# Kernel optimization log

Measured on AMD Instinct MI355X. Metric: run time of the kernel, lower is better.

The kernel has to match this reference:

```python
import jax, jax.numpy as jnp
import numpy as np

NUM_USERS = 100000
NUM_ITEMS = 50000
NUM_EDGES = 1000000
H = 64            # initial embedding dim
DIMS = [64, 64]   # per-layer output dims
B = 16384         # BPR batch size
NEG_SLOPE = 0.2
EPS = 1e-12


def setup_inputs() -> dict:
    key = jax.random.key(0)
    ks = jax.random.split(key, 20)
    s = 1.0 / np.sqrt(H)
    inp = {
        'user_emb': jax.random.normal(ks[0], (NUM_USERS, H), jnp.float32) * 0.1,
        'item_emb': jax.random.normal(ks[1], (NUM_ITEMS, H), jnp.float32) * 0.1,
        'W1_0': jax.random.normal(ks[2], (H, DIMS[0]), jnp.float32) * s,
        'b1_0': jnp.zeros((DIMS[0],), jnp.float32),
        'W2_0': jax.random.normal(ks[3], (H, DIMS[0]), jnp.float32) * s,
        'b2_0': jnp.zeros((DIMS[0],), jnp.float32),
        'W1_1': jax.random.normal(ks[4], (DIMS[0], DIMS[1]), jnp.float32) * s,
        'b1_1': jnp.zeros((DIMS[1],), jnp.float32),
        'W2_1': jax.random.normal(ks[5], (DIMS[0], DIMS[1]), jnp.float32) * s,
        'b2_1': jnp.zeros((DIMS[1],), jnp.float32),
        'edge_index': jnp.stack([
            jax.random.randint(ks[6], (NUM_EDGES,), 0, NUM_USERS),
            jax.random.randint(ks[7], (NUM_EDGES,), 0, NUM_ITEMS),
        ], axis=0),
        'users': jax.random.randint(ks[8], (B,), 0, NUM_USERS),
        'pos_items': jax.random.randint(ks[9], (B,), 0, NUM_ITEMS),
        'neg_items': jax.random.randint(ks[10], (B,), 0, NUM_ITEMS),
    }
    return inp


def _edge_norm(src, dst):
    # symmetric sqrt-degree norm: (deg_src * deg_dst) ** -0.5 per edge
    ones = jnp.ones(src.shape[0], jnp.float32)
    du = jax.ops.segment_sum(ones, src, num_segments=NUM_USERS)[src]
    di = jax.ops.segment_sum(ones, dst, num_segments=NUM_ITEMS)[dst]
    return ((du * di) ** -0.5)[:, None]  # [E, 1]


def _epilogue(h):
    # leaky_relu(0.2) -> (dropout eval = identity) -> L2 row-normalize
    h = jnp.where(h >= 0, h, NEG_SLOPE * h)
    n = jnp.sqrt(jnp.sum(h * h, axis=1, keepdims=True))
    return h / jnp.maximum(n, EPS)


def _layer(u, i, src, dst, norm, W1, b1, W2, b2):
    # node-level W1 transform, gathered per edge (same math as per-edge W1(x_j))
    u1 = u @ W1 + b1            # [Nu, d]
    i1 = i @ W1 + b1            # [Ni, d]
    cross = u[src] * i[dst]     # [E, din]  shared by both directions
    mW2 = cross @ W2 + b2       # [E, d]
    # user -> item: x_j = user[src], aggregate at item dst
    out_i = jax.ops.segment_sum(norm * u1[src] + mW2, dst, num_segments=NUM_ITEMS)
    # item -> user: x_j = item[dst], aggregate at user src
    out_u = jax.ops.segment_sum(norm * i1[dst] + mW2, src, num_segments=NUM_USERS)
    return _epilogue(out_u), _epilogue(out_i)


def reference(user_emb, item_emb, W1_0, b1_0, W2_0, b2_0, W1_1, b1_1, W2_1, b2_1,
              edge_index, users, pos_items, neg_items):
    src, dst = edge_index[0], edge_index[1]
    norm = _edge_norm(src, dst)
    u_list, i_list = [user_emb], [item_emb]
    u, i = user_emb, item_emb
    u, i = _layer(u, i, src, dst, norm, W1_0, b1_0, W2_0, b2_0)
    u_list.append(u); i_list.append(i)
    u, i = _layer(u, i, src, dst, norm, W1_1, b1_1, W2_1, b2_1)
    u_list.append(u); i_list.append(i)
    user_all = jnp.concatenate(u_list, axis=1)   # [Nu, H+sum(DIMS)]
    item_all = jnp.concatenate(i_list, axis=1)   # [Ni, H+sum(DIMS)]
    return (user_all[users], item_all[pos_items], item_all[neg_items])
```

## Files before the change

### kernel.cpp

```cpp
#include <hip/hip_runtime.h>

#define NU 100000
#define NI 50000
#define NE 1000000
#define NB 16384

#define UB ((NU + 1023) / 1024)
#define IB ((NI + 1023) / 1024)

__global__ void deg_kernel(const int* __restrict__ ei, int* du, int* di) {
    int e = blockIdx.x * blockDim.x + threadIdx.x;
    if (e >= NE) return;
    atomicAdd(&du[ei[e]], 1);
    atomicAdd(&di[ei[NE + e]], 1);
}

__global__ __launch_bounds__(1024) void scan1_kernel(
        const int* __restrict__ du, const int* __restrict__ di,
        int* __restrict__ psum, float* __restrict__ rsd_u, float* __restrict__ rsd_i) {
    int b = blockIdx.x, tid = threadIdx.x;
    int v = 0;
    if (b < UB) {
        int i = b * 1024 + tid;
        if (i < NU) {
            int d = du[i]; v = d;
            rsd_u[i] = d > 0 ? 1.0f / sqrtf((float)d) : 0.f;
        }
    } else {
        int i = (b - UB) * 1024 + tid;
        if (i < NI) {
            int d = di[i]; v = d;
            rsd_i[i] = d > 0 ? 1.0f / sqrtf((float)d) : 0.f;
        }
    }
    int s = v;
    #pragma unroll
    for (int off = 32; off > 0; off >>= 1) s += __shfl_xor(s, off);
    __shared__ int ws[16];
    if ((tid & 63) == 0) ws[tid >> 6] = s;
    __syncthreads();
    if (tid == 0) {
        int t = 0;
        #pragma unroll
        for (int w = 0; w < 16; ++w) t += ws[w];
        psum[b] = t;
    }
}

__global__ __launch_bounds__(128) void scan2_kernel(int* __restrict__ psum) {
    int base = (blockIdx.x == 0) ? 0 : UB;
    int n = (blockIdx.x == 0) ? UB : IB;
    int tid = threadIdx.x;
    __shared__ int sh[128];
    int v = (tid < n) ? psum[base + tid] : 0;
    sh[tid] = v;
    __syncthreads();
    for (int off = 1; off < 128; off <<= 1) {
        int t = (tid >= off) ? sh[tid - off] : 0;
        __syncthreads();
        sh[tid] += t;
        __syncthreads();
    }
    if (tid < n) psum[base + tid] = sh[tid] - v;
}

__global__ __launch_bounds__(1024) void scan3_kernel(
        const int* __restrict__ du, const int* __restrict__ di,
        const int* __restrict__ psum,
        int* __restrict__ rp_u, int* __restrict__ rp_i,
        int* __restrict__ cur_u, int* __restrict__ cur_i) {
    int b = blockIdx.x, tid = threadIdx.x;
    const int* deg; int* rp; int* cur; int N; int i0;
    if (b < UB) { deg = du; rp = rp_u; cur = cur_u; N = NU; i0 = b * 1024; }
    else        { deg = di; rp = rp_i; cur = cur_i; N = NI; i0 = (b - UB) * 1024; }
    int i = i0 + tid;
    int v = (i < N) ? deg[i] : 0;
    __shared__ int sh[1024];
    sh[tid] = v;
    __syncthreads();
    for (int off = 1; off < 1024; off <<= 1) {
        int t = (tid >= off) ? sh[tid - off] : 0;
        __syncthreads();
        sh[tid] += t;
        __syncthreads();
    }
    int excl = sh[tid] - v + psum[b];
    if (i < N) { rp[i] = excl; cur[i] = excl; }
    if (b == 0 && tid == 0) { rp_u[NU] = NE; rp_i[NI] = NE; }
}

__global__ void fill_csr_kernel(const int* __restrict__ ei,
                                int* __restrict__ curu, int* __restrict__ curi,
                                int* __restrict__ csr_u, int* __restrict__ csr_i) {
    int e = blockIdx.x * blockDim.x + threadIdx.x;
    if (e >= NE) return;
    int s = ei[e], d = ei[NE + e];
    int si = atomicAdd(&curi[d], 1);
    csr_i[si] = s;
    int su = atomicAdd(&curu[s], 1);
    csr_u[su] = d;
}

__global__ __launch_bounds__(512) void gt_fused_kernel(
        const float* __restrict__ xu, const float* __restrict__ xi,
        const int* __restrict__ rpu, const int* __restrict__ rpi,
        const int* __restrict__ csru, const int* __restrict__ csri,
        const float* __restrict__ rsdu, const float* __restrict__ rsdi,
        const float* __restrict__ W1, const float* __restrict__ b1,
        const float* __restrict__ W2, const float* __restrict__ b2,
        float* __restrict__ outu, float* __restrict__ outi) {
    __shared__ float w1s[64 * 64];
    __shared__ float w2s[64 * 64];
    __shared__ float acs[8][128];
    int tid = threadIdx.x;
    #pragma unroll
    for (int t = 0; t < 8; ++t) {
        w1s[t * 512 + tid] = W1[t * 512 + tid];
        w2s[t * 512 + tid] = W2[t * 512 + tid];
    }
    __syncthreads();
    int wv = tid >> 6, lane = tid & 63;
    float b1v = b1[lane], b2v = b2[lane];
    const int NG = (NI + NU + 7) / 8;
    for (int g = blockIdx.x; g < NG; g += gridDim.x) {
        int n = g * 8 + wv;
        bool act = n < NI + NU;
        bool isItem = n < NI;
        int nn = isItem ? n : n - NI;
        const int* rp   = isItem ? rpi : rpu;
        const int* cs   = isItem ? csri : csru;
        const float* xin  = isItem ? xi : xu;
        const float* embo = isItem ? xu : xi;
        const float* rso  = isItem ? rsdu : rsdi;
        const float* rown = isItem ? rsdi : rsdu;
        float* outp = isItem ? outi : outu;

        float sp = 0.f, ss = 0.f, sw = 0.f, rs = 0.f, dgf = 0.f, xv = 0.f;
        if (act) {
            int beg = rp[nn], end = rp[nn + 1];
            dgf = (float)(end - beg);
            rs = rown[nn];
            xv = xin[nn * 64 + lane];
            int j = beg;
            for (; j + 3 < end; j += 4) {
                int i0 = cs[j], i1 = cs[j + 1], i2 = cs[j + 2], i3 = cs[j + 3];
                float w0 = rso[i0], w1v = rso[i1], w2v = rso[i2], w3v = rso[i3];
                float v0 = embo[i0 * 64 + lane];
                float v1 = embo[i1 * 64 + lane];
                float v2 = embo[i2 * 64 + lane];
                float v3 = embo[i3 * 64 + lane];
                sp += (v0 + v1) + (v2 + v3);
                ss += w0 * v0 + w1v * v1 + w2v * v2 + w3v * v3;
                sw += (w0 + w1v) + (w2v + w3v);
            }
            for (; j < end; ++j) {
                int i0 = cs[j];
                float w0 = rso[i0];
                float v0 = embo[i0 * 64 + lane];
                sp += v0; ss += w0 * v0; sw += w0;
            }
        }
        acs[wv][lane] = rs * ss;
        acs[wv][64 + lane] = xv * sp;
        if (act) {
            float acc = 0.f;
            #pragma unroll 8
            for (int k = 0; k < 64; ++k) {
                acc += acs[wv][k] * w1s[k * 64 + lane];
                acc += acs[wv][64 + k] * w2s[k * 64 + lane];
            }
            acc += rs * sw * b1v + dgf * b2v;
            float h = acc >= 0.f ? acc : 0.2f * acc;
            float nsq = h * h;
            #pragma unroll
            for (int off = 32; off > 0; off >>= 1) nsq += __shfl_xor(nsq, off);
            float nrm = sqrtf(nsq);
            outp[nn * 64 + lane] = h / fmaxf(nrm, 1e-12f);
        }
    }
}

__global__ void gather_kernel(const float* __restrict__ ue, const float* __restrict__ u1,
                              const float* __restrict__ u2, const float* __restrict__ ie,
                              const float* __restrict__ i1, const float* __restrict__ i2,
                              const int* __restrict__ users, const int* __restrict__ pos,
                              const int* __restrict__ neg, float* __restrict__ out) {
    int idx = blockIdx.x * blockDim.x + threadIdx.x;
    if (idx >= 3 * NB * 192) return;
    int which = idx / (NB * 192);
    int rem = idx - which * (NB * 192);
    int b = rem / 192, c = rem - b * 192;
    int seg = c >> 6, cc = c & 63;
    int row;
    const float* srcarr;
    if (which == 0) {
        row = users[b];
        srcarr = (seg == 0) ? ue : (seg == 1 ? u1 : u2);
    } else {
        row = (which == 1) ? pos[b] : neg[b];
        srcarr = (seg == 0) ? ie : (seg == 1 ? i1 : i2);
    }
    out[idx] = srcarr[(size_t)row * 64 + cc];
}

extern "C" void kernel_launch(void* const* d_in, const int* in_sizes, int n_in,
                              void* d_out, int out_size, void* d_ws, size_t ws_size,
                              hipStream_t stream) {
    const float* user_emb = (const float*)d_in[0];
    const float* item_emb = (const float*)d_in[1];
    const float* W1_0 = (const float*)d_in[2];
    const float* b1_0 = (const float*)d_in[3];
    const float* W2_0 = (const float*)d_in[4];
    const float* b2_0 = (const float*)d_in[5];
    const float* W1_1 = (const float*)d_in[6];
    const float* b1_1 = (const float*)d_in[7];
    const float* W2_1 = (const float*)d_in[8];
    const float* b2_1 = (const float*)d_in[9];
    const int* ei = (const int*)d_in[10];
    const int* users = (const int*)d_in[11];
    const int* pos = (const int*)d_in[12];
    const int* neg = (const int*)d_in[13];
    float* out = (float*)d_out;

    char* p = (char*)d_ws;
    int* du = (int*)p;        p += NU * 4;
    int* di = (int*)p;        p += NI * 4;
    float* rsd_u = (float*)p; p += NU * 4;
    float* rsd_i = (float*)p; p += NI * 4;
    int* psum = (int*)p;      p += (UB + IB) * 4;
    int* rp_u = (int*)p;      p += (NU + 1) * 4;
    int* rp_i = (int*)p;      p += (NI + 1) * 4;
    int* cur_u = (int*)p;     p += NU * 4;
    int* cur_i = (int*)p;     p += NI * 4;
    int* csr_u = (int*)p;     p += (size_t)NE * 4;
    int* csr_i = (int*)p;     p += (size_t)NE * 4;
    float* u1 = (float*)p;    p += (size_t)NU * 64 * 4;
    float* u2 = (float*)p;    p += (size_t)NU * 64 * 4;
    float* i1 = (float*)p;    p += (size_t)NI * 64 * 4;
    float* i2 = (float*)p;    p += (size_t)NI * 64 * 4;

    hipMemsetAsync(du, 0, (size_t)(NU + NI) * sizeof(int), stream);

    deg_kernel<<<(NE + 255) / 256, 256, 0, stream>>>(ei, du, di);
    scan1_kernel<<<UB + IB, 1024, 0, stream>>>(du, di, psum, rsd_u, rsd_i);
    scan2_kernel<<<2, 128, 0, stream>>>(psum);
    scan3_kernel<<<UB + IB, 1024, 0, stream>>>(du, di, psum, rp_u, rp_i, cur_u, cur_i);
    fill_csr_kernel<<<(NE + 255) / 256, 256, 0, stream>>>(ei, cur_u, cur_i, csr_u, csr_i);

    gt_fused_kernel<<<1280, 512, 0, stream>>>(user_emb, item_emb, rp_u, rp_i, csr_u, csr_i,
                                              rsd_u, rsd_i, W1_0, b1_0, W2_0, b2_0, u1, i1);
    gt_fused_kernel<<<1280, 512, 0, stream>>>(u1, i1, rp_u, rp_i, csr_u, csr_i,
                                              rsd_u, rsd_i, W1_1, b1_1, W2_1, b2_1, u2, i2);

    gather_kernel<<<(3 * NB * 192 + 255) / 256, 256, 0, stream>>>(
        user_emb, u1, u2, item_emb, i1, i2, users, pos, neg, out);
}
```

Baseline: 709.5 us.

## Batch four nodes per wavefront with transposed swizzled weights and vectorized gather

Each wavefront now aggregates four nodes before the dense transform. The 64x64 weights are stored transposed in shared memory with an XOR swizzle, so each lane reads its output column as float4 and reuses it across the four nodes. This cuts LDS traffic in the matmul, at the cost of more registers and serialized neighbor gathers per wave. The grid grows to 2048 blocks, and the final gather copies float4 instead of scalars.

```diff
diff --git a/kernel.cpp b/kernel.cpp
--- a/kernel.cpp
+++ b/kernel.cpp
@@ -101,6 +101,7 @@
     csr_u[su] = d;
 }
 
+#define BATCH 4
 __global__ __launch_bounds__(512) void gt_fused_kernel(
         const float* __restrict__ xu, const float* __restrict__ xi,
         const int* __restrict__ rpu, const int* __restrict__ rpi,
@@ -109,68 +110,91 @@
         const float* __restrict__ W1, const float* __restrict__ b1,
         const float* __restrict__ W2, const float* __restrict__ b2,
         float* __restrict__ outu, float* __restrict__ outi) {
-    __shared__ float w1s[64 * 64];
-    __shared__ float w2s[64 * 64];
-    __shared__ float acs[8][128];
+    __shared__ float wt1[64 * 64];
+    __shared__ float wt2[64 * 64];
+    __shared__ float acs[8][BATCH][128];
     int tid = threadIdx.x;
     #pragma unroll
-    for (int t = 0; t < 8; ++t) {
-        w1s[t * 512 + tid] = W1[t * 512 + tid];
-        w2s[t * 512 + tid] = W2[t * 512 + tid];
+    for (int r = 0; r < 8; ++r) {
+        int e = r * 512 + tid;
+        int k = e >> 6, d = e & 63;
+        int dst = d * 64 + (((k >> 2) ^ (d & 7)) << 2) + (k & 3);
+        wt1[dst] = W1[e];
+        wt2[dst] = W2[e];
     }
     __syncthreads();
     int wv = tid >> 6, lane = tid & 63;
     float b1v = b1[lane], b2v = b2[lane];
-    const int NG = (NI + NU + 7) / 8;
+    int wrow = lane * 64;
+    const int NG = (NI + NU + 31) / 32;
     for (int g = blockIdx.x; g < NG; g += gridDim.x) {
-        int n = g * 8 + wv;
-        bool act = n < NI + NU;
-        bool isItem = n < NI;
-        int nn = isItem ? n : n - NI;
-        const int* rp   = isItem ? rpi : rpu;
-        const int* cs   = isItem ? csri : csru;
-        const float* xin  = isItem ? xi : xu;
-        const float* embo = isItem ? xu : xi;
-        const float* rso  = isItem ? rsdu : rsdi;
-        const float* rown = isItem ? rsdi : rsdu;
-        float* outp = isItem ? outi : outu;
-
-        float sp = 0.f, ss = 0.f, sw = 0.f, rs = 0.f, dgf = 0.f, xv = 0.f;
-        if (act) {
-            int beg = rp[nn], end = rp[nn + 1];
-            dgf = (float)(end - beg);
-            rs = rown[nn];
-            xv = xin[nn * 64 + lane];
-            int j = beg;
-            for (; j + 3 < end; j += 4) {
-                int i0 = cs[j], i1 = cs[j + 1], i2 = cs[j + 2], i3 = cs[j + 3];
-                float w0 = rso[i0], w1v = rso[i1], w2v = rso[i2], w3v = rso[i3];
-                float v0 = embo[i0 * 64 + lane];
-                float v1 = embo[i1 * 64 + lane];
-                float v2 = embo[i2 * 64 + lane];
-                float v3 = embo[i3 * 64 + lane];
-                sp += (v0 + v1) + (v2 + v3);
-                ss += w0 * v0 + w1v * v1 + w2v * v2 + w3v * v3;
-                sw += (w0 + w1v) + (w2v + w3v);
+        int nbase = g * 32 + wv * BATCH;
+        float ba[BATCH], dg[BATCH];
+        #pragma unroll
+        for (int j = 0; j < BATCH; ++j) {
+            int n = nbase + j;
+            bool act = n < NI + NU;
+            bool isItem = n < NI;
+            int nn = isItem ? n : n - NI;
+            const int* rp     = isItem ? rpi : rpu;
+            const int* cs     = isItem ? csri : csru;
+            const float* xin  = isItem ? xi : xu;
+            const float* embo = isItem ? xu : xi;
+            const float* rso  = isItem ? rsdu : rsdi;
+            const float* rown = isItem ? rsdi : rsdu;
+            float sp = 0.f, ss = 0.f, sw = 0.f, rs = 0.f, dgf = 0.f, xv = 0.f;
+            if (act) {
+                int beg = rp[nn], end = rp[nn + 1];
+                dgf = (float)(end - beg);
+                rs = rown[nn];
+                xv = xin[nn * 64 + lane];
+                int jj = beg;
+                for (; jj + 3 < end; jj += 4) {
+                    int i0 = cs[jj], i1 = cs[jj + 1], i2 = cs[jj + 2], i3 = cs[jj + 3];
+                    float w0 = rso[i0], w1v = rso[i1], w2v = rso[i2], w3v = rso[i3];
+                    float v0 = embo[i0 * 64 + lane];
+                    float v1 = embo[i1 * 64 + lane];
+                    float v2 = embo[i2 * 64 + lane];
+                    float v3 = embo[i3 * 64 + lane];
+                    sp += (v0 + v1) + (v2 + v3);
+                    ss += w0 * v0 + w1v * v1 + w2v * v2 + w3v * v3;
+                    sw += (w0 + w1v) + (w2v + w3v);
+                }
+                for (; jj < end; ++jj) {
+                    int i0 = cs[jj];
+                    float w0 = rso[i0];
+                    float v0 = embo[i0 * 64 + lane];
+                    sp += v0; ss += w0 * v0; sw += w0;
+                }
             }
-            for (; j < end; ++j) {
-                int i0 = cs[j];
-                float w0 = rso[i0];
-                float v0 = embo[i0 * 64 + lane];
-                sp += v0; ss += w0 * v0; sw += w0;
+            ba[j] = rs * sw;
+            dg[j] = dgf;
+            acs[wv][j][lane] = rs * ss;
+            acs[wv][j][64 + lane] = xv * sp;
+        }
+        float acc[BATCH] = {0.f, 0.f, 0.f, 0.f};
+        int sw8 = (lane & 7);
+        #pragma unroll 4
+        for (int c = 0; c < 16; ++c) {
+            float4 w1v = *(const float4*)&wt1[wrow + ((c ^ sw8) << 2)];
+            float4 w2v = *(const float4*)&wt2[wrow + ((c ^ sw8) << 2)];
+            #pragma unroll
+            for (int j = 0; j < BATCH; ++j) {
+                float4 av = *(const float4*)&acs[wv][j][c * 4];
+                float4 cv = *(const float4*)&acs[wv][j][64 + c * 4];
+                acc[j] += av.x * w1v.x + av.y * w1v.y + av.z * w1v.z + av.w * w1v.w
+                        + cv.x * w2v.x + cv.y * w2v.y + cv.z * w2v.z + cv.w * w2v.w;
             }
         }
-        acs[wv][lane] = rs * ss;
-        acs[wv][64 + lane] = xv * sp;
-        if (act) {
-            float acc = 0.f;
-            #pragma unroll 8
-            for (int k = 0; k < 64; ++k) {
-                acc += acs[wv][k] * w1s[k * 64 + lane];
-                acc += acs[wv][64 + k] * w2s[k * 64 + lane];
-            }
-            acc += rs * sw * b1v + dgf * b2v;
-            float h = acc >= 0.f ? acc : 0.2f * acc;
+        #pragma unroll
+        for (int j = 0; j < BATCH; ++j) {
+            int n = nbase + j;
+            if (n >= NI + NU) continue;
+            bool isItem = n < NI;
+            int nn = isItem ? n : n - NI;
+            float* outp = isItem ? outi : outu;
+            float h = acc[j] + ba[j] * b1v + dg[j] * b2v;
+            h = h >= 0.f ? h : 0.2f * h;
             float nsq = h * h;
             #pragma unroll
             for (int off = 32; off > 0; off >>= 1) nsq += __shfl_xor(nsq, off);
@@ -184,13 +208,13 @@
                               const float* __restrict__ u2, const float* __restrict__ ie,
                               const float* __restrict__ i1, const float* __restrict__ i2,
                               const int* __restrict__ users, const int* __restrict__ pos,
-                              const int* __restrict__ neg, float* __restrict__ out) {
+                              const int* __restrict__ neg, float4* __restrict__ out) {
     int idx = blockIdx.x * blockDim.x + threadIdx.x;
-    if (idx >= 3 * NB * 192) return;
-    int which = idx / (NB * 192);
-    int rem = idx - which * (NB * 192);
-    int b = rem / 192, c = rem - b * 192;
-    int seg = c >> 6, cc = c & 63;
+    if (idx >= 3 * NB * 48) return;
+    int which = idx / (NB * 48);
+    int rem = idx - which * (NB * 48);
+    int b = rem / 48, c4 = rem - b * 48;
+    int seg = c4 >> 4, cc = (c4 & 15) << 2;
     int row;
     const float* srcarr;
     if (which == 0) {
@@ -200,7 +224,7 @@
         row = (which == 1) ? pos[b] : neg[b];
         srcarr = (seg == 0) ? ie : (seg == 1 ? i1 : i2);
     }
-    out[idx] = srcarr[(size_t)row * 64 + cc];
+    out[idx] = *(const float4*)&srcarr[(size_t)row * 64 + cc];
 }
 
 extern "C" void kernel_launch(void* const* d_in, const int* in_sizes, int n_in,
@@ -220,7 +244,6 @@
     const int* users = (const int*)d_in[11];
     const int* pos = (const int*)d_in[12];
     const int* neg = (const int*)d_in[13];
-    float* out = (float*)d_out;
 
     char* p = (char*)d_ws;
     int* du = (int*)p;        p += NU * 4;
@@ -247,11 +270,11 @@
     scan3_kernel<<<UB + IB, 1024, 0, stream>>>(du, di, psum, rp_u, rp_i, cur_u, cur_i);
     fill_csr_kernel<<<(NE + 255) / 256, 256, 0, stream>>>(ei, cur_u, cur_i, csr_u, csr_i);
 
-    gt_fused_kernel<<<1280, 512, 0, stream>>>(user_emb, item_emb, rp_u, rp_i, csr_u, csr_i,
+    gt_fused_kernel<<<2048, 512, 0, stream>>>(user_emb, item_emb, rp_u, rp_i, csr_u, csr_i,
                                               rsd_u, rsd_i, W1_0, b1_0, W2_0, b2_0, u1, i1);
-    gt_fused_kernel<<<1280, 512, 0, stream>>>(u1, i1, rp_u, rp_i, csr_u, csr_i,
+    gt_fused_kernel<<<2048, 512, 0, stream>>>(u1, i1, rp_u, rp_i, csr_u, csr_i,
                                               rsd_u, rsd_i, W1_1, b1_1, W2_1, b2_1, u2, i2);
 
-    gather_kernel<<<(3 * NB * 192 + 255) / 256, 256, 0, stream>>>(
-        user_emb, u1, u2, item_emb, i1, i2, users, pos, neg, out);
-}
+    gather_kernel<<<(3 * NB * 48 + 255) / 256, 256, 0, stream>>>(
+        user_emb, u1, u2, item_emb, i1, i2, users, pos, neg, (float4*)d_out);
+}
```

Result: slower. 1.073 ms (+51.3%).
